# Kernel optimization log

Measured on AMD Instinct MI355X. Metric: run time of the kernel, lower is better.

## Reference

```python
import jax, jax.numpy as jnp
import numpy as np

B, S, D_IN = 2, 2048, 2048
H, KVH, HD = 32, 8, 64
GROUPS = H // KVH
EPS = 1e-6
SCALE = HD ** -0.5


def setup_inputs() -> dict:
    key = jax.random.key(0)
    ks = jax.random.split(key, 6)
    x = jax.random.normal(ks[0], (B, S, D_IN), jnp.float32)
    Wq = jax.random.normal(ks[1], (H * HD, D_IN), jnp.float32) * 0.02
    Wk = jax.random.normal(ks[2], (KVH * HD, D_IN), jnp.float32) * 0.02
    Wv = jax.random.normal(ks[3], (KVH * HD, D_IN), jnp.float32) * 0.02
    Wo = jax.random.normal(ks[4], (D_IN, H * HD), jnp.float32) * 0.02
    w_qnorm = jnp.ones((HD,), jnp.float32)
    w_knorm = jnp.ones((HD,), jnp.float32)
    # Llama-style RoPE tables: [S, HD] with frequencies duplicated across halves
    inv_freq = 1.0 / (10000.0 ** (np.arange(0, HD, 2, dtype=np.float32) / HD))
    ang = np.outer(np.arange(S, dtype=np.float32), inv_freq)  # [S, HD/2]
    emb = np.concatenate([ang, ang], axis=-1)  # [S, HD]
    cos = jnp.asarray(np.cos(emb), jnp.float32)
    sin = jnp.asarray(np.sin(emb), jnp.float32)
    mask = jnp.tril(jnp.ones((S, S), jnp.bool_))  # unused by module (causal hardcoded)
    return dict(x=x, mask=mask, cos=cos, sin=sin, Wq=Wq, Wk=Wk, Wv=Wv, Wo=Wo,
                w_qnorm=w_qnorm, w_knorm=w_knorm)


def _rms_norm(t, w):
    # per-head-dim RMSNorm, eps inside sqrt (torch nn.RMSNorm semantics)
    var = jnp.mean(jnp.square(t), axis=-1, keepdims=True)
    return t * jax.lax.rsqrt(var + EPS) * w


def _rotate_half(t):
    t1, t2 = jnp.split(t, 2, axis=-1)
    return jnp.concatenate([-t2, t1], axis=-1)


def _rope(t, cos, sin):
    # t: [B,H,S,HD]; cos/sin: [S,HD]
    return t * cos[None, None] + _rotate_half(t) * sin[None, None]


def reference(x, mask, cos, sin, Wq, Wk, Wv, Wo, w_qnorm, w_knorm):
    bs, seq, _ = x.shape
    q = (x @ Wq.T).reshape(bs, seq, H, HD).transpose(0, 2, 1, 3)    # [B,H,S,hd]
    k = (x @ Wk.T).reshape(bs, seq, KVH, HD).transpose(0, 2, 1, 3)  # [B,KVH,S,hd]
    v = (x @ Wv.T).reshape(bs, seq, KVH, HD).transpose(0, 2, 1, 3)
    # GQA: repeat_interleave KV over head dim
    k = jnp.repeat(k, GROUPS, axis=1)
    v = jnp.repeat(v, GROUPS, axis=1)
    # fused QK RMSNorm then RoPE
    q = _rope(_rms_norm(q, w_qnorm), cos, sin)
    k = _rope(_rms_norm(k, w_knorm), cos, sin)
    # causal attention
    scores = jnp.einsum('bhqd,bhkd->bhqk', q, k) * SCALE
    causal = jnp.arange(seq)[:, None] >= jnp.arange(seq)[None, :]
    scores = jnp.where(causal, scores, jnp.finfo(scores.dtype).min)
    attn = jax.nn.softmax(scores, axis=-1)
    out = jnp.einsum('bhqk,bhkd->bhqd', attn, v)
    out = out.transpose(0, 2, 1, 3).reshape(bs, seq, H * HD)
    return out @ Wo.T
```

## Files before the change

### kernel.cpp

```cpp
#include <hip/hip_runtime.h>

typedef __bf16 bf16_t;
typedef __bf16 bf16x8 __attribute__((ext_vector_type(8)));
typedef __bf16 bf16x4 __attribute__((ext_vector_type(4)));
typedef float f32x4 __attribute__((ext_vector_type(4)));
typedef unsigned int u32;

#define AS1 __attribute__((address_space(1)))
#define AS3 __attribute__((address_space(3)))

#define ASTR 72

#if __has_builtin(__builtin_amdgcn_exp2f)
#define EXP2(x) __builtin_amdgcn_exp2f(x)
#else
#define EXP2(x) exp2f(x)
#endif

__device__ __forceinline__ void g2l16(const bf16_t* g, bf16_t* l) {
  __builtin_amdgcn_global_load_lds((const AS1 u32*)g, (AS3 u32*)l, 16, 0, 0);
}

__device__ __forceinline__ u32 pkbf(float a, float b) {
  u32 ua = __builtin_bit_cast(u32, a) + 0x8000u;
  u32 ub = __builtin_bit_cast(u32, b) + 0x8000u;
  return (ua >> 16) | (ub & 0xFFFF0000u);
}

__global__ __launch_bounds__(256) void cvt5(
    const float* __restrict__ s0, const float* __restrict__ s1,
    const float* __restrict__ s2, const float* __restrict__ s3,
    const float* __restrict__ s4,
    bf16_t* __restrict__ d0, bf16_t* __restrict__ d1, bf16_t* __restrict__ d2,
    bf16_t* __restrict__ d3, bf16_t* __restrict__ d4)
{
  int blk = blockIdx.x;
  const float* s; bf16_t* d; int off;
  if      (blk <  8192) { s = s0; d = d0; off = blk;         }
  else if (blk < 12288) { s = s1; d = d1; off = blk -  8192; }
  else if (blk < 13312) { s = s2; d = d2; off = blk - 12288; }
  else if (blk < 14336) { s = s3; d = d3; off = blk - 13312; }
  else                  { s = s4; d = d4; off = blk - 14336; }
  size_t i = (size_t)off * 1024 + threadIdx.x * 4;
  float4 v = *(const float4*)&s[i];
  bf16x4 t;
  t[0] = (bf16_t)v.x; t[1] = (bf16_t)v.y; t[2] = (bf16_t)v.z; t[3] = (bf16_t)v.w;
  *(bf16x4*)&d[i] = t;
}

__device__ __forceinline__ void gemm_core(
    const bf16_t* __restrict__ A, const bf16_t* __restrict__ B, int K,
    bf16_t* AsL, bf16_t* AsH, bf16_t* BsL, bf16_t* BsH, f32x4 (&acc)[4][4])
{
  const int tid = threadIdx.x, lane = tid & 63, w = tid >> 6;
  const int col = lane & 15, quad = lane >> 4;
  const int wm = w >> 1, wn = w & 1;
  const int lr = lane >> 2;
  const int lc = (((lane & 3) ^ ((lane >> 3) & 3)) << 3);
  const int sw = ((quad ^ ((col >> 1) & 3)) << 3);
  const bf16_t* ga = A + (size_t)(w * 16 + lr) * K + lc;
  const bf16_t* gb = B + (size_t)(w * 16 + lr) * K + lc;
  const int lo0 = (w * 16) * 32, lo1 = (64 + w * 16) * 32;

  const int nkb = K >> 6;
  for (int kb = 0; kb < nkb; ++kb) {
    const int kbase = kb * 64;
    __syncthreads();
    g2l16(ga + kbase,                     AsL + lo0);
    g2l16(ga + kbase + 32,                AsH + lo0);
    g2l16(ga + kbase + (size_t)64 * K,      AsL + lo1);
    g2l16(ga + kbase + (size_t)64 * K + 32, AsH + lo1);
    g2l16(gb + kbase,                     BsL + lo0);
    g2l16(gb + kbase + 32,                BsH + lo0);
    g2l16(gb + kbase + (size_t)64 * K,      BsL + lo1);
    g2l16(gb + kbase + (size_t)64 * K + 32, BsH + lo1);
    __syncthreads();

#pragma unroll
    for (int kk = 0; kk < 2; ++kk) {
      const bf16_t* Ah = kk ? AsH : AsL;
      const bf16_t* Bh = kk ? BsH : BsL;
      bf16x8 af[4], bfr[4];
#pragma unroll
      for (int mt = 0; mt < 4; ++mt)
        af[mt] = *(const bf16x8*)&Ah[(wm * 64 + mt * 16 + col) * 32 + sw];
#pragma unroll
      for (int nt = 0; nt < 4; ++nt)
        bfr[nt] = *(const bf16x8*)&Bh[(wn * 64 + nt * 16 + col) * 32 + sw];
#pragma unroll
      for (int mt = 0; mt < 4; ++mt)
#pragma unroll
        for (int nt = 0; nt < 4; ++nt)
          acc[mt][nt] = __builtin_amdgcn_mfma_f32_16x16x32_bf16(af[mt], bfr[nt], acc[mt][nt], 0, 0, 0);
    }
  }
}

__global__ __launch_bounds__(256, 3) void gemm_qkv(
    const bf16_t* __restrict__ xb, const bf16_t* __restrict__ Wqb,
    const bf16_t* __restrict__ Wkb, const bf16_t* __restrict__ Wvb,
    const float* __restrict__ cosT, const float* __restrict__ sinT,
    const float* __restrict__ wq, const float* __restrict__ wk,
    bf16_t* __restrict__ Qn, bf16_t* __restrict__ Kn, bf16_t* __restrict__ Vp)
{
  __shared__ bf16_t AsL[128 * 32], AsH[128 * 32], BsL[128 * 32], BsH[128 * 32];
  const int bn = blockIdx.x, bm = blockIdx.y;
  const bf16_t* B;
  if      (bn < 16) B = Wqb + (size_t)bn * 128 * 2048;
  else if (bn < 20) B = Wkb + (size_t)(bn - 16) * 128 * 2048;
  else              B = Wvb + (size_t)(bn - 20) * 128 * 2048;

  f32x4 acc[4][4] = {};
  gemm_core(xb + (size_t)bm * 128 * 2048, B, 2048, AsL, AsH, BsL, BsH, acc);

  const int lane = threadIdx.x & 63, w = threadIdx.x >> 6;
  const int col = lane & 15, quad = lane >> 4, wm = w >> 1, wn = w & 1;

  if (bn < 20) {
    const bool isQ = bn < 16;
    const float* wnv = isQ ? wq : wk;
    float w4[4];
#pragma unroll
    for (int nt = 0; nt < 4; ++nt) w4[nt] = wnv[nt * 16 + col];
    bf16_t* dst = isQ ? Qn + ((size_t)(bn * 2 + wn)) * 2048 * 64
                      : Kn + ((size_t)((bn - 16) * 2 + wn)) * 2048 * 64;
    const size_t bstride = isQ ? (size_t)32 * 2048 * 64 : (size_t)8 * 2048 * 64;
    const float qscale = 0.125f * 1.4426950408889634f;

#pragma unroll
    for (int mt = 0; mt < 4; ++mt)
#pragma unroll
      for (int r = 0; r < 4; ++r) {
        int row = bm * 128 + wm * 64 + mt * 16 + quad * 4 + r;
        int b = row >> 11, s = row & 2047;
        float v[4], ss = 0.f;
#pragma unroll
        for (int nt = 0; nt < 4; ++nt) { v[nt] = acc[mt][nt][r]; ss += v[nt] * v[nt]; }
        ss += __shfl_xor(ss, 1, 64);
        ss += __shfl_xor(ss, 2, 64);
        ss += __shfl_xor(ss, 4, 64);
        ss += __shfl_xor(ss, 8, 64);
        float rr = rsqrtf(ss * (1.0f / 64.0f) + 1e-6f);
        float t[4];
#pragma unroll
        for (int nt = 0; nt < 4; ++nt) t[nt] = v[nt] * rr * w4[nt];
        bf16_t* drow = dst + b * bstride + (size_t)s * 64;
#pragma unroll
        for (int nt = 0; nt < 4; ++nt) {
          int hd = nt * 16 + col;
          float rot = (nt < 2) ? -t[nt + 2] : t[nt - 2];
          float ov = t[nt] * cosT[s * 64 + hd] + rot * sinT[s * 64 + hd];
          if (isQ) ov *= qscale;
          drow[hd] = (bf16_t)ov;
        }
      }
  } else {
    const int cb = (bn - 20) * 128;
#pragma unroll
    for (int mt = 0; mt < 4; ++mt)
#pragma unroll
      for (int r = 0; r < 4; ++r) {
        int row = bm * 128 + wm * 64 + mt * 16 + quad * 4 + r;
        bf16_t* crow = Vp + (size_t)row * 512 + cb + wn * 64 + col;
#pragma unroll
        for (int nt = 0; nt < 4; ++nt)
          crow[nt * 16] = (bf16_t)acc[mt][nt][r];
      }
  }
}

__global__ __launch_bounds__(256, 3) void gemm_o(
    const bf16_t* __restrict__ Ao, const bf16_t* __restrict__ Wob,
    float* __restrict__ Cf)
{
  __shared__ bf16_t AsL[128 * 32], AsH[128 * 32], BsL[128 * 32], BsH[128 * 32];
  const int bn = blockIdx.x, bm = blockIdx.y;
  f32x4 acc[4][4] = {};
  gemm_core(Ao + (size_t)bm * 128 * 2048, Wob + (size_t)bn * 128 * 2048, 2048,
            AsL, AsH, BsL, BsH, acc);

  const int lane = threadIdx.x & 63, w = threadIdx.x >> 6;
  const int col = lane & 15, quad = lane >> 4, wm = w >> 1, wn = w & 1;
#pragma unroll
  for (int mt = 0; mt < 4; ++mt)
#pragma unroll
    for (int r = 0; r < 4; ++r) {
      int row = bm * 128 + wm * 64 + mt * 16 + quad * 4 + r;
      float* crow = Cf + (size_t)row * 2048 + bn * 128 + wn * 64 + col;
#pragma unroll
      for (int nt = 0; nt < 4; ++nt)
        crow[nt * 16] = acc[mt][nt][r];
    }
}

__global__ __launch_bounds__(256) void vtrans(
    const bf16_t* __restrict__ Vp, bf16_t* __restrict__ Vt)
{
  __shared__ bf16_t T[64 * 136];
  const int st = blockIdx.x, kvh = blockIdx.y, b = blockIdx.z;
  const int tid = threadIdx.x;
#pragma unroll
  for (int p = 0; p < 4; ++p) {
    int r = p * 32 + (tid >> 3);
    int c = (tid & 7) * 8;
    bf16x8 v = *(const bf16x8*)&Vp[((size_t)(b * 2048 + st * 128 + r)) * 512 + kvh * 64 + c];
#pragma unroll
    for (int i = 0; i < 8; ++i) T[(c + i) * 136 + r] = v[i];
  }
  __syncthreads();
#pragma unroll
  for (int p = 0; p < 4; ++p) {
    int hd = p * 16 + (tid >> 4);
    int sc = (tid & 15) * 8;
    bf16x8 v = *(const bf16x8*)&T[hd * 136 + sc];
    *(bf16x8*)&Vt[((size_t)((b * 8 + kvh) * 64) + hd) * 2048 + st * 128 + sc] = v;
  }
}

__global__ __launch_bounds__(256, 4) void attn(
    const bf16_t* __restrict__ Qn, const bf16_t* __restrict__ Kn,
    const bf16_t* __restrict__ Vt, bf16_t* __restrict__ Ao)
{
  __shared__ bf16_t KsL[64 * 32], KsH[64 * 32];
  __shared__ bf16_t VsL[64 * 32], VsH[64 * 32];
  __shared__ bf16_t Ps[128 * ASTR];

  const int tid = threadIdx.x, lane = tid & 63, w = tid >> 6;
  const int col = lane & 15, quad = lane >> 4;
  const int lr = lane >> 2;
  const int lcs = (((lane & 3) ^ ((lane >> 3) & 3)) << 3);
  const int sw  = ((quad ^ ((col >> 1) & 3)) << 3);
  const int pair = blockIdx.x;
  const int h = blockIdx.y, b = blockIdx.z;
  const int kvh = h >> 2;

  const bf16_t* Kb = Kn + ((size_t)(b * 8 + kvh)) * 2048 * 64;
  const bf16_t* Vb = Vt + ((size_t)(b * 8 + kvh)) * 64 * 2048;
  bf16_t* lKL = KsL + w * 512;
  bf16_t* lKH = KsH + w * 512;
  bf16_t* lVL = VsL + w * 512;
  bf16_t* lVH = VsH + w * 512;

  bf16x8 ones;
#pragma unroll
  for (int i = 0; i < 8; ++i) ones[i] = (bf16_t)1.0f;

#pragma unroll
  for (int ph = 0; ph < 2; ++ph) {
    const int qt = ph ? (15 - pair) : pair;
    const bf16_t* Qb = Qn + (((size_t)(b * 32 + h)) * 2048 + qt * 128) * 64;

    bf16x8 Qf[2][2];
#pragma unroll
    for (int mt = 0; mt < 2; ++mt)
#pragma unroll
      for (int kk = 0; kk < 2; ++kk)
        Qf[mt][kk] = *(const bf16x8*)&Qb[(w * 32 + mt * 16 + col) * 64 + kk * 32 + quad * 8];

    f32x4 o[2][4] = {};
    f32x4 lacc[2] = {};

    const int rowmin = qt * 128 + w * 32;
    const int rowmax = rowmin + 31;
    const int jmax = 2 * qt + 1;

    for (int j = 0; j <= jmax; ++j) {
      __syncthreads();
      {
        const bf16_t* gk = &Kb[(size_t)(j * 64 + w * 16 + lr) * 64 + lcs];
        const bf16_t* gv = &Vb[(size_t)(w * 16 + lr) * 2048 + j * 64 + lcs];
        g2l16(gk,      lKL);
        g2l16(gk + 32, lKH);
        g2l16(gv,      lVL);
        g2l16(gv + 32, lVH);
      }
      __syncthreads();

      if (j * 64 <= rowmax) {
        const bool needmask = (j * 64 + 63 > rowmin);

#pragma unroll
        for (int kt = 0; kt < 4; ++kt) {
          bf16x8 kf0 = *(const bf16x8*)&KsL[(kt * 16 + col) * 32 + sw];
          bf16x8 kf1 = *(const bf16x8*)&KsH[(kt * 16 + col) * 32 + sw];
          f32x4 st0 = {}, st1 = {};
          st0 = __builtin_amdgcn_mfma_f32_16x16x32_bf16(kf0, Qf[0][0], st0, 0, 0, 0);
          st0 = __builtin_amdgcn_mfma_f32_16x16x32_bf16(kf1, Qf[0][1], st0, 0, 0, 0);
          st1 = __builtin_amdgcn_mfma_f32_16x16x32_bf16(kf0, Qf[1][0], st1, 0, 0, 0);
          st1 = __builtin_amdgcn_mfma_f32_16x16x32_bf16(kf1, Qf[1][1], st1, 0, 0, 0);
          const int k0 = j * 64 + kt * 16 + quad * 4;
#pragma unroll
          for (int mt = 0; mt < 2; ++mt) {
            f32x4 st = mt ? st1 : st0;
            float p0 = EXP2(st[0]), p1 = EXP2(st[1]);
            float p2 = EXP2(st[2]), p3 = EXP2(st[3]);
            if (needmask) {
              const int qg = qt * 128 + w * 32 + mt * 16 + col;
              p0 = (k0 + 0 > qg) ? 0.f : p0;
              p1 = (k0 + 1 > qg) ? 0.f : p1;
              p2 = (k0 + 2 > qg) ? 0.f : p2;
              p3 = (k0 + 3 > qg) ? 0.f : p3;
            }
            uint2 pk = { pkbf(p0, p1), pkbf(p2, p3) };
            *(uint2*)&Ps[(w * 32 + mt * 16 + col) * ASTR + kt * 16 + quad * 4] = pk;
          }
        }
        asm volatile("s_waitcnt lgkmcnt(0)" ::: "memory");

#pragma unroll
        for (int kk = 0; kk < 2; ++kk) {
          const bf16_t* Vh = kk ? VsH : VsL;
          bf16x8 pa0 = *(const bf16x8*)&Ps[(w * 32 + col) * ASTR + kk * 32 + quad * 8];
          bf16x8 pa1 = *(const bf16x8*)&Ps[(w * 32 + 16 + col) * ASTR + kk * 32 + quad * 8];
          lacc[0] = __builtin_amdgcn_mfma_f32_16x16x32_bf16(pa0, ones, lacc[0], 0, 0, 0);
          lacc[1] = __builtin_amdgcn_mfma_f32_16x16x32_bf16(pa1, ones, lacc[1], 0, 0, 0);
#pragma unroll
          for (int nt = 0; nt < 4; ++nt) {
            bf16x8 vf = *(const bf16x8*)&Vh[(nt * 16 + col) * 32 + sw];
            o[0][nt] = __builtin_amdgcn_mfma_f32_16x16x32_bf16(pa0, vf, o[0][nt], 0, 0, 0);
            o[1][nt] = __builtin_amdgcn_mfma_f32_16x16x32_bf16(pa1, vf, o[1][nt], 0, 0, 0);
          }
        }
      }
    }

#pragma unroll
    for (int mt = 0; mt < 2; ++mt)
#pragma unroll
      for (int r = 0; r < 4; ++r) {
        float inv = 1.0f / lacc[mt][r];
        int row = b * 2048 + qt * 128 + w * 32 + mt * 16 + quad * 4 + r;
        bf16_t* orow = &Ao[(size_t)row * 2048 + h * 64 + col];
#pragma unroll
        for (int nt = 0; nt < 4; ++nt)
          orow[nt * 16] = (bf16_t)(o[mt][nt][r] * inv);
      }
  }
}

extern "C" void kernel_launch(void* const* d_in, const int* in_sizes, int n_in,
                              void* d_out, int out_size, void* d_ws, size_t ws_size,
                              hipStream_t stream)
{
  const float* x    = (const float*)d_in[0];
  const float* cosT = (const float*)d_in[2];
  const float* sinT = (const float*)d_in[3];
  const float* Wq   = (const float*)d_in[4];
  const float* Wk   = (const float*)d_in[5];
  const float* Wv   = (const float*)d_in[6];
  const float* Wo   = (const float*)d_in[7];
  const float* wq   = (const float*)d_in[8];
  const float* wk   = (const float*)d_in[9];
  float* out = (float*)d_out;

  char* ws = (char*)d_ws;
  bf16_t* xb  = (bf16_t*)(ws);
  bf16_t* Ao  = (bf16_t*)(ws);
  bf16_t* Wqb = (bf16_t*)(ws + 16777216);
  bf16_t* Vt  = (bf16_t*)(ws + 16777216);
  bf16_t* Wkb = (bf16_t*)(ws + 25165824);
  bf16_t* Wvb = (bf16_t*)(ws + 27262976);
  bf16_t* Wob = (bf16_t*)(ws + 29360128);
  bf16_t* Vp  = (bf16_t*)(ws + 37748736);
  bf16_t* Qn  = (bf16_t*)(ws + 41943040);
  bf16_t* Kn  = (bf16_t*)(ws + 58720256);

  cvt5<<<18432, 256, 0, stream>>>(x, Wq, Wk, Wv, Wo, xb, Wqb, Wkb, Wvb, Wob);
  gemm_qkv<<<dim3(24, 32), 256, 0, stream>>>(xb, Wqb, Wkb, Wvb, cosT, sinT, wq, wk, Qn, Kn, Vp);
  vtrans<<<dim3(16, 8, 2), 256, 0, stream>>>(Vp, Vt);
  attn<<<dim3(8, 32, 2), 256, 0, stream>>>(Qn, Kn, Vt, Ao);
  gemm_o<<<dim3(16, 32), 256, 0, stream>>>(Ao, Wob, out);
}
```

Before: 305.4 us.

## Double-buffer K/V tiles in attention and launch one block per query tile

The attention kernel now double-buffers the K and V shared-memory tiles, issuing the async global-to-LDS load for the next key block before computing on the current one. This removes one barrier per iteration and is meant to overlap load latency with the MFMA work. The paired-tile scheme (each block handled tile p and 15-p) is replaced by one block per query tile, with the heaviest tiles launched first via qt = 15 - blockIdx.z, which doubles the grid and relies on the scheduler for load balance. In exchange, LDS use per block grows and the occupancy hint drops from 4 to 3 blocks.

```diff
diff --git a/kernel.cpp b/kernel.cpp
--- a/kernel.cpp
+++ b/kernel.cpp
@@ -217,12 +217,12 @@
   }
 }
 
-__global__ __launch_bounds__(256, 4) void attn(
+__global__ __launch_bounds__(256, 3) void attn(
     const bf16_t* __restrict__ Qn, const bf16_t* __restrict__ Kn,
     const bf16_t* __restrict__ Vt, bf16_t* __restrict__ Ao)
 {
-  __shared__ bf16_t KsL[64 * 32], KsH[64 * 32];
-  __shared__ bf16_t VsL[64 * 32], VsH[64 * 32];
+  __shared__ bf16_t KsL[2][64 * 32], KsH[2][64 * 32];
+  __shared__ bf16_t VsL[2][64 * 32], VsH[2][64 * 32];
   __shared__ bf16_t Ps[128 * ASTR];
 
   const int tid = threadIdx.x, lane = tid & 63, w = tid >> 6;
@@ -230,112 +230,114 @@
   const int lr = lane >> 2;
   const int lcs = (((lane & 3) ^ ((lane >> 3) & 3)) << 3);
   const int sw  = ((quad ^ ((col >> 1) & 3)) << 3);
-  const int pair = blockIdx.x;
-  const int h = blockIdx.y, b = blockIdx.z;
+  const int h = blockIdx.x, b = blockIdx.y;
+  const int qt = 15 - blockIdx.z;
   const int kvh = h >> 2;
 
   const bf16_t* Kb = Kn + ((size_t)(b * 8 + kvh)) * 2048 * 64;
   const bf16_t* Vb = Vt + ((size_t)(b * 8 + kvh)) * 64 * 2048;
-  bf16_t* lKL = KsL + w * 512;
-  bf16_t* lKH = KsH + w * 512;
-  bf16_t* lVL = VsL + w * 512;
-  bf16_t* lVH = VsH + w * 512;
+  const bf16_t* Qb = Qn + (((size_t)(b * 32 + h)) * 2048 + qt * 128) * 64;
+  const int lw = w * 512;
+
+  bf16x8 Qf[2][2];
+#pragma unroll
+  for (int mt = 0; mt < 2; ++mt)
+#pragma unroll
+    for (int kk = 0; kk < 2; ++kk)
+      Qf[mt][kk] = *(const bf16x8*)&Qb[(w * 32 + mt * 16 + col) * 64 + kk * 32 + quad * 8];
 
   bf16x8 ones;
 #pragma unroll
   for (int i = 0; i < 8; ++i) ones[i] = (bf16_t)1.0f;
 
-#pragma unroll
-  for (int ph = 0; ph < 2; ++ph) {
-    const int qt = ph ? (15 - pair) : pair;
-    const bf16_t* Qb = Qn + (((size_t)(b * 32 + h)) * 2048 + qt * 128) * 64;
-
-    bf16x8 Qf[2][2];
-#pragma unroll
-    for (int mt = 0; mt < 2; ++mt)
-#pragma unroll
-      for (int kk = 0; kk < 2; ++kk)
-        Qf[mt][kk] = *(const bf16x8*)&Qb[(w * 32 + mt * 16 + col) * 64 + kk * 32 + quad * 8];
-
-    f32x4 o[2][4] = {};
-    f32x4 lacc[2] = {};
-
-    const int rowmin = qt * 128 + w * 32;
-    const int rowmax = rowmin + 31;
-    const int jmax = 2 * qt + 1;
-
-    for (int j = 0; j <= jmax; ++j) {
-      __syncthreads();
-      {
-        const bf16_t* gk = &Kb[(size_t)(j * 64 + w * 16 + lr) * 64 + lcs];
-        const bf16_t* gv = &Vb[(size_t)(w * 16 + lr) * 2048 + j * 64 + lcs];
-        g2l16(gk,      lKL);
-        g2l16(gk + 32, lKH);
-        g2l16(gv,      lVL);
-        g2l16(gv + 32, lVH);
-      }
-      __syncthreads();
-
-      if (j * 64 <= rowmax) {
-        const bool needmask = (j * 64 + 63 > rowmin);
-
-#pragma unroll
-        for (int kt = 0; kt < 4; ++kt) {
-          bf16x8 kf0 = *(const bf16x8*)&KsL[(kt * 16 + col) * 32 + sw];
-          bf16x8 kf1 = *(const bf16x8*)&KsH[(kt * 16 + col) * 32 + sw];
-          f32x4 st0 = {}, st1 = {};
-          st0 = __builtin_amdgcn_mfma_f32_16x16x32_bf16(kf0, Qf[0][0], st0, 0, 0, 0);
-          st0 = __builtin_amdgcn_mfma_f32_16x16x32_bf16(kf1, Qf[0][1], st0, 0, 0, 0);
-          st1 = __builtin_amdgcn_mfma_f32_16x16x32_bf16(kf0, Qf[1][0], st1, 0, 0, 0);
-          st1 = __builtin_amdgcn_mfma_f32_16x16x32_bf16(kf1, Qf[1][1], st1, 0, 0, 0);
-          const int k0 = j * 64 + kt * 16 + quad * 4;
-#pragma unroll
-          for (int mt = 0; mt < 2; ++mt) {
-            f32x4 st = mt ? st1 : st0;
-            float p0 = EXP2(st[0]), p1 = EXP2(st[1]);
-            float p2 = EXP2(st[2]), p3 = EXP2(st[3]);
-            if (needmask) {
-              const int qg = qt * 128 + w * 32 + mt * 16 + col;
-              p0 = (k0 + 0 > qg) ? 0.f : p0;
-              p1 = (k0 + 1 > qg) ? 0.f : p1;
-              p2 = (k0 + 2 > qg) ? 0.f : p2;
-              p3 = (k0 + 3 > qg) ? 0.f : p3;
-            }
-            uint2 pk = { pkbf(p0, p1), pkbf(p2, p3) };
-            *(uint2*)&Ps[(w * 32 + mt * 16 + col) * ASTR + kt * 16 + quad * 4] = pk;
+  f32x4 o[2][4] = {};
+  f32x4 lacc[2] = {};
+
+  const int rowmin = qt * 128 + w * 32;
+  const int rowmax = rowmin + 31;
+  const int jmax = 2 * qt + 1;
+
+  {
+    const bf16_t* gk = &Kb[(size_t)(w * 16 + lr) * 64 + lcs];
+    const bf16_t* gv = &Vb[(size_t)(w * 16 + lr) * 2048 + lcs];
+    g2l16(gk,      &KsL[0][lw]);
+    g2l16(gk + 32, &KsH[0][lw]);
+    g2l16(gv,      &VsL[0][lw]);
+    g2l16(gv + 32, &VsH[0][lw]);
+  }
+
+  for (int j = 0; j <= jmax; ++j) {
+    __syncthreads();
+    if (j < jmax) {
+      const int nb = (j + 1) & 1;
+      const bf16_t* gk = &Kb[(size_t)((j + 1) * 64 + w * 16 + lr) * 64 + lcs];
+      const bf16_t* gv = &Vb[(size_t)(w * 16 + lr) * 2048 + (j + 1) * 64 + lcs];
+      g2l16(gk,      &KsL[nb][lw]);
+      g2l16(gk + 32, &KsH[nb][lw]);
+      g2l16(gv,      &VsL[nb][lw]);
+      g2l16(gv + 32, &VsH[nb][lw]);
+    }
+
+    if (j * 64 <= rowmax) {
+      const int bf = j & 1;
+      const bool needmask = (j * 64 + 63 > rowmin);
+
+#pragma unroll
+      for (int kt = 0; kt < 4; ++kt) {
+        bf16x8 kf0 = *(const bf16x8*)&KsL[bf][(kt * 16 + col) * 32 + sw];
+        bf16x8 kf1 = *(const bf16x8*)&KsH[bf][(kt * 16 + col) * 32 + sw];
+        f32x4 st0 = {}, st1 = {};
+        st0 = __builtin_amdgcn_mfma_f32_16x16x32_bf16(kf0, Qf[0][0], st0, 0, 0, 0);
+        st0 = __builtin_amdgcn_mfma_f32_16x16x32_bf16(kf1, Qf[0][1], st0, 0, 0, 0);
+        st1 = __builtin_amdgcn_mfma_f32_16x16x32_bf16(kf0, Qf[1][0], st1, 0, 0, 0);
+        st1 = __builtin_amdgcn_mfma_f32_16x16x32_bf16(kf1, Qf[1][1], st1, 0, 0, 0);
+        const int k0 = j * 64 + kt * 16 + quad * 4;
+#pragma unroll
+        for (int mt = 0; mt < 2; ++mt) {
+          f32x4 st = mt ? st1 : st0;
+          float p0 = EXP2(st[0]), p1 = EXP2(st[1]);
+          float p2 = EXP2(st[2]), p3 = EXP2(st[3]);
+          if (needmask) {
+            const int qg = qt * 128 + w * 32 + mt * 16 + col;
+            p0 = (k0 + 0 > qg) ? 0.f : p0;
+            p1 = (k0 + 1 > qg) ? 0.f : p1;
+            p2 = (k0 + 2 > qg) ? 0.f : p2;
+            p3 = (k0 + 3 > qg) ? 0.f : p3;
           }
-        }
-        asm volatile("s_waitcnt lgkmcnt(0)" ::: "memory");
-
-#pragma unroll
-        for (int kk = 0; kk < 2; ++kk) {
-          const bf16_t* Vh = kk ? VsH : VsL;
-          bf16x8 pa0 = *(const bf16x8*)&Ps[(w * 32 + col) * ASTR + kk * 32 + quad * 8];
-          bf16x8 pa1 = *(const bf16x8*)&Ps[(w * 32 + 16 + col) * ASTR + kk * 32 + quad * 8];
-          lacc[0] = __builtin_amdgcn_mfma_f32_16x16x32_bf16(pa0, ones, lacc[0], 0, 0, 0);
-          lacc[1] = __builtin_amdgcn_mfma_f32_16x16x32_bf16(pa1, ones, lacc[1], 0, 0, 0);
-#pragma unroll
-          for (int nt = 0; nt < 4; ++nt) {
-            bf16x8 vf = *(const bf16x8*)&Vh[(nt * 16 + col) * 32 + sw];
-            o[0][nt] = __builtin_amdgcn_mfma_f32_16x16x32_bf16(pa0, vf, o[0][nt], 0, 0, 0);
-            o[1][nt] = __builtin_amdgcn_mfma_f32_16x16x32_bf16(pa1, vf, o[1][nt], 0, 0, 0);
-          }
+          uint2 pk = { pkbf(p0, p1), pkbf(p2, p3) };
+          *(uint2*)&Ps[(w * 32 + mt * 16 + col) * ASTR + kt * 16 + quad * 4] = pk;
         }
       }
-    }
-
-#pragma unroll
-    for (int mt = 0; mt < 2; ++mt)
-#pragma unroll
-      for (int r = 0; r < 4; ++r) {
-        float inv = 1.0f / lacc[mt][r];
-        int row = b * 2048 + qt * 128 + w * 32 + mt * 16 + quad * 4 + r;
-        bf16_t* orow = &Ao[(size_t)row * 2048 + h * 64 + col];
-#pragma unroll
-        for (int nt = 0; nt < 4; ++nt)
-          orow[nt * 16] = (bf16_t)(o[mt][nt][r] * inv);
+      asm volatile("s_waitcnt lgkmcnt(0)" ::: "memory");
+
+#pragma unroll
+      for (int kk = 0; kk < 2; ++kk) {
+        const bf16_t* Vh = kk ? &VsH[bf][0] : &VsL[bf][0];
+        bf16x8 pa0 = *(const bf16x8*)&Ps[(w * 32 + col) * ASTR + kk * 32 + quad * 8];
+        bf16x8 pa1 = *(const bf16x8*)&Ps[(w * 32 + 16 + col) * ASTR + kk * 32 + quad * 8];
+        lacc[0] = __builtin_amdgcn_mfma_f32_16x16x32_bf16(pa0, ones, lacc[0], 0, 0, 0);
+        lacc[1] = __builtin_amdgcn_mfma_f32_16x16x32_bf16(pa1, ones, lacc[1], 0, 0, 0);
+#pragma unroll
+        for (int nt = 0; nt < 4; ++nt) {
+          bf16x8 vf = *(const bf16x8*)&Vh[(nt * 16 + col) * 32 + sw];
+          o[0][nt] = __builtin_amdgcn_mfma_f32_16x16x32_bf16(pa0, vf, o[0][nt], 0, 0, 0);
+          o[1][nt] = __builtin_amdgcn_mfma_f32_16x16x32_bf16(pa1, vf, o[1][nt], 0, 0, 0);
+        }
       }
-  }
+    }
+  }
+
+#pragma unroll
+  for (int mt = 0; mt < 2; ++mt)
+#pragma unroll
+    for (int r = 0; r < 4; ++r) {
+      float inv = 1.0f / lacc[mt][r];
+      int row = b * 2048 + qt * 128 + w * 32 + mt * 16 + quad * 4 + r;
+      bf16_t* orow = &Ao[(size_t)row * 2048 + h * 64 + col];
+#pragma unroll
+      for (int nt = 0; nt < 4; ++nt)
+        orow[nt * 16] = (bf16_t)(o[mt][nt][r] * inv);
+    }
 }
 
 extern "C" void kernel_launch(void* const* d_in, const int* in_sizes, int n_in,
@@ -368,6 +370,6 @@
   cvt5<<<18432, 256, 0, stream>>>(x, Wq, Wk, Wv, Wo, xb, Wqb, Wkb, Wvb, Wob);
   gemm_qkv<<<dim3(24, 32), 256, 0, stream>>>(xb, Wqb, Wkb, Wvb, cosT, sinT, wq, wk, Qn, Kn, Vp);
   vtrans<<<dim3(16, 8, 2), 256, 0, stream>>>(Vp, Vt);
-  attn<<<dim3(8, 32, 2), 256, 0, stream>>>(Qn, Kn, Vt, Ao);
+  attn<<<dim3(32, 2, 16), 256, 0, stream>>>(Qn, Kn, Vt, Ao);
   gemm_o<<<dim3(16, 32), 256, 0, stream>>>(Ao, Wob, out);
 }
```

Result: faster. 298.2 us (-2.3%).
